# Kernel optimization log

Hardware: AMD Instinct MI355X
Metric: run time of the kernel (lower is better)

Reference implementation:

```python
import jax, jax.numpy as jnp
import numpy as np

HIDDEN = 256
OUT_CH = 3
OMEGA_0 = 30.0
PATCH = 5


def setup_inputs() -> dict:
    key = jax.random.key(0)
    ks = jax.random.split(key, 9)
    B, C, H, W = 1, 128, 256, 256
    in_dim = C * PATCH * PATCH + 2  # 3202
    xi = jax.random.normal(ks[0], (B, C, H, W), dtype=jnp.float32)

    def lin(kw, kb, fi, fo):
        s = 1.0 / np.sqrt(fi)
        Wm = jax.random.uniform(kw, (fi, fo), jnp.float32, -s, s)
        bm = jax.random.uniform(kb, (fo,), jnp.float32, -s, s)
        return Wm, bm

    W1, b1 = lin(ks[1], ks[2], in_dim, HIDDEN)
    W2, b2 = lin(ks[3], ks[4], HIDDEN, HIDDEN)
    W3, b3 = lin(ks[5], ks[6], HIDDEN, HIDDEN)
    W4, b4 = lin(ks[7], ks[8], HIDDEN, OUT_CH)
    return {"xi": xi, "W1": W1, "b1": b1, "W2": W2, "b2": b2,
            "W3": W3, "b3": b3, "W4": W4, "b4": b4}


def _make_coords(B, H, W, dtype):
    # normalized pixel coords in [-1, 1], shape [B*H*W, 2]
    ys = jnp.linspace(-1.0, 1.0, H, dtype=dtype)
    xs = jnp.linspace(-1.0, 1.0, W, dtype=dtype)
    gy, gx = jnp.meshgrid(ys, xs, indexing="ij")
    coords = jnp.stack([gy, gx], axis=-1).reshape(H * W, 2)
    return jnp.tile(coords, (B, 1))


def reference(xi, W1, b1, W2, b2, W3, b3, W4, b4):
    B, C, H, W = xi.shape
    # im2col 5x5 patch gather (zero pad), like F.unfold with padding=2
    patches = jax.lax.conv_general_dilated_patches(
        xi, (PATCH, PATCH), (1, 1), "SAME")  # [B, C*25, H, W]
    feat = jnp.transpose(patches, (0, 2, 3, 1)).reshape(B * H * W, C * PATCH * PATCH)
    coords = _make_coords(B, H, W, xi.dtype)
    x = jnp.concatenate([feat, coords], axis=-1)  # [N, 3202]
    h = jnp.sin(OMEGA_0 * (x @ W1 + b1))
    h = jnp.sin(OMEGA_0 * (h @ W2 + b2))
    h = jnp.sin(OMEGA_0 * (h @ W3 + b3))
    out = h @ W4 + b4  # [N, 3]
    rgb = out.reshape(B, H, W, OUT_CH).transpose(0, 3, 1, 2)
    return rgb
```

## Files before the change

kernel.cpp:

```cpp
#include <hip/hip_runtime.h>
#include <math.h>
#include <stdint.h>

typedef _Float16 f16;
typedef _Float16 f16x8 __attribute__((ext_vector_type(8)));
typedef float f32x4 __attribute__((ext_vector_type(4)));
typedef unsigned short u16;
typedef u16 u16x8 __attribute__((ext_vector_type(8)));

#define HID 256
#define NS1C 100
#define NS2 8
#define NPX 65536
#define BPXG 256
#define NBG (NPX/BPXG)
#define SPAD 260
#define NSP (SPAD*SPAD)

#define OFF_W1C 0
#define SZ_W1C  ((size_t)NS1C*32768)
#define OFF_W2  SZ_W1C
#define SZ_W2   ((size_t)NS2*32768)
#define OFF_W3  (OFF_W2+SZ_W2)
#define OFF_XH  ((size_t)4194304)
#define SZ_XP   ((size_t)NSP*128*2)
#define OFF_XL  (OFF_XH + SZ_XP)
#define OFF_HH  (OFF_XL + SZ_XP)
#define SZ_HP   ((size_t)NPX*HID*2)
#define OFF_HL  (OFF_HH + SZ_HP)

__device__ inline void split2(float v, u16& h, u16& l){
  f16 hv = (f16)v;
  f16 lv = (f16)(v - (float)hv);
  h = __builtin_bit_cast(u16, hv);
  l = __builtin_bit_cast(u16, lv);
}

__global__ void prep_w(const float* __restrict__ W, int Kact, int nStages,
                       u16* __restrict__ outp){
  int t = blockIdx.x*256 + threadIdx.x;
  if (t >= nStages*1024) return;
  int s = t >> 10, r = t & 1023;
  int w = r >> 8, nf = (r >> 6) & 3, l = r & 63;
  int col = w*64 + nf*16 + (l & 15);
  int kb  = s*32 + (l >> 4)*8;
  u16x8 hv, lv;
  #pragma unroll
  for (int j = 0; j < 8; ++j){
    int k = kb + j;
    float v = (k < Kact) ? W[(size_t)k*HID + col] : 0.f;
    u16 h, lo; split2(v, h, lo);
    hv[j] = h; lv[j] = lo;
  }
  size_t U0 = ((((size_t)s*4 + w)*4 + nf)*2 + 0)*64 + l;
  *(u16x8*)(outp + U0*8)      = hv;
  *(u16x8*)(outp + (U0+64)*8) = lv;
}

__global__ void prep_w1c(const float* __restrict__ W1, u16* __restrict__ outp){
  int t = blockIdx.x*256 + threadIdx.x;
  if (t >= NS1C*1024) return;
  int s = t >> 10, r = t & 1023;
  int w = r >> 8, nf = (r >> 6) & 3, l = r & 63;
  int col = w*64 + nf*16 + (l & 15);
  int tap = s >> 2, cg = s & 3;
  int cb  = cg*32 + (l >> 4)*8;
  u16x8 hv, lv;
  #pragma unroll
  for (int j = 0; j < 8; ++j){
    int c = cb + j;
    float v = W1[(size_t)(c*25 + tap)*HID + col];
    u16 h, lo; split2(v, h, lo);
    hv[j] = h; lv[j] = lo;
  }
  size_t U0 = ((((size_t)s*4 + w)*4 + nf)*2 + 0)*64 + l;
  *(u16x8*)(outp + U0*8)      = hv;
  *(u16x8*)(outp + (U0+64)*8) = lv;
}

__global__ __launch_bounds__(256)
void prep_x(const float* __restrict__ xi, u16* __restrict__ Xh, u16* __restrict__ Xl){
  int sp = blockIdx.x*256 + threadIdx.x;
  if (sp >= NSP) return;
  int py = sp / SPAD;
  int px = sp - py*SPAD;
  bool inb = (py >= 2) & (py < 258) & (px >= 2) & (px < 258);
  const float* xin = xi + ((size_t)(py-2)<<8) + (px-2);
  #pragma unroll 4
  for (int cg = 0; cg < 16; ++cg){
    u16x8 hv, lv;
    #pragma unroll
    for (int j = 0; j < 8; ++j){
      float v = inb ? xin[((size_t)(cg*8 + j))<<16] : 0.f;
      u16 h, l; split2(v, h, l); hv[j] = h; lv[j] = l;
    }
    *(u16x8*)(Xh + (size_t)sp*128 + cg*8) = hv;
    *(u16x8*)(Xl + (size_t)sp*128 + cg*8) = lv;
  }
}

template<int MODE>
__global__ __launch_bounds__(512, 2)
void gemm(const u16* __restrict__ Ah, const u16* __restrict__ Al,
          const u16* __restrict__ Wp, const float* __restrict__ W1,
          const float* __restrict__ bias, u16* __restrict__ Hh, u16* __restrict__ Hl,
          const float* __restrict__ W4, const float* __restrict__ b4,
          float* __restrict__ out, int nt)
{
  __shared__ __align__(16) u16 Sb[65536];

  const int tid  = threadIdx.x;
  const int lane = tid & 63;
  const int wv   = tid >> 6;
  const int wm   = wv >> 2, wn = wv & 3;

  int bid = blockIdx.x;
  bid = (bid & 7)*(NBG/8) + (bid >> 3);
  const int pxb = bid * BPXG;
  const int y   = bid;

  f32x4 acc[8][4];
  #pragma unroll
  for (int a=0;a<8;a++)
    #pragma unroll
    for (int bq=0;bq<4;bq++) acc[a][bq] = f32x4{0.f,0.f,0.f,0.f};

#define A_STAGE(S, BUF) do { \
    _Pragma("unroll") \
    for (int u=0;u<2;++u){ \
      const int mfb = wv*2 + u; \
      size_t off; \
      if (MODE == 0){ \
        const int tap = (S) >> 2, cg = (S) & 3; \
        const int dy = tap/5, dx = tap - 5*dy; \
        const int sp = (y + dy)*SPAD + dx + mfb*16 + (lane & 15); \
        off = (size_t)sp*128 + cg*32 + (lane >> 4)*8; \
      } else { \
        const int px = pxb + mfb*16 + (lane & 15); \
        off = (size_t)px*HID + (S)*32 + (lane >> 4)*8; \
      } \
      __builtin_amdgcn_global_load_lds( \
        (const __attribute__((address_space(1))) uint32_t*)(Ah + off), \
        (__attribute__((address_space(3))) uint32_t*)((char*)Sb + (size_t)(BUF)*32768 + (mfb*2+0)*1024), \
        16, 0, 0); \
      __builtin_amdgcn_global_load_lds( \
        (const __attribute__((address_space(1))) uint32_t*)(Al + off), \
        (__attribute__((address_space(3))) uint32_t*)((char*)Sb + (size_t)(BUF)*32768 + (mfb*2+1)*1024), \
        16, 0, 0); \
    } \
  } while(0)

#define B_STAGE(S, BUF) do { \
    const char* _src = (const char*)Wp + (size_t)(S)*32768 + wv*4096 + lane*16; \
    char* _dst = (char*)Sb + 65536 + (size_t)(BUF)*32768 + wv*4096; \
    _Pragma("unroll") \
    for (int i=0;i<4;++i) \
      __builtin_amdgcn_global_load_lds( \
        (const __attribute__((address_space(1))) uint32_t*)(_src + i*1024), \
        (__attribute__((address_space(3))) uint32_t*)(_dst + i*1024), 16, 0, 0); \
  } while(0)

  A_STAGE(0, 0); B_STAGE(0, 0);

  for (int t = 0; t < nt; ++t){
    asm volatile("s_waitcnt vmcnt(0)" ::: "memory");
    __builtin_amdgcn_s_barrier();
    __builtin_amdgcn_sched_barrier(0);
    const int cur = t & 1;
    if (t+1 < nt){
      A_STAGE(t+1, cur^1);
      B_STAGE(t+1, cur^1);
    }

    const u16* Abuf = (const u16*)Sb + (size_t)cur*16384;
    const u16* Bbuf = (const u16*)Sb + 32768 + (size_t)cur*16384;

    f16x8 bh[4], bl[4];
    #pragma unroll
    for (int nf=0;nf<4;++nf){
      bh[nf] = *(const f16x8*)(Bbuf + ((size_t)((wn*4+nf)*2+0)*64 + lane)*8);
      bl[nf] = *(const f16x8*)(Bbuf + ((size_t)((wn*4+nf)*2+1)*64 + lane)*8);
    }
    __builtin_amdgcn_s_setprio(1);
    #pragma unroll
    for (int hf=0; hf<2; ++hf){
      f16x8 ahv[4], alv[4];
      #pragma unroll
      for (int m=0;m<4;++m){
        const int mfb = wm*8 + hf*4 + m;
        ahv[m] = *(const f16x8*)(Abuf + ((size_t)(mfb*2+0)*64 + lane)*8);
        alv[m] = *(const f16x8*)(Abuf + ((size_t)(mfb*2+1)*64 + lane)*8);
      }
      #pragma unroll
      for (int m=0;m<4;++m)
        #pragma unroll
        for (int nf=0;nf<4;++nf)
          acc[hf*4+m][nf] = __builtin_amdgcn_mfma_f32_16x16x32_f16(ahv[m], bh[nf], acc[hf*4+m][nf], 0,0,0);
      #pragma unroll
      for (int m=0;m<4;++m)
        #pragma unroll
        for (int nf=0;nf<4;++nf)
          acc[hf*4+m][nf] = __builtin_amdgcn_mfma_f32_16x16x32_f16(alv[m], bh[nf], acc[hf*4+m][nf], 0,0,0);
      #pragma unroll
      for (int m=0;m<4;++m)
        #pragma unroll
        for (int nf=0;nf<4;++nf)
          acc[hf*4+m][nf] = __builtin_amdgcn_mfma_f32_16x16x32_f16(ahv[m], bl[nf], acc[hf*4+m][nf], 0,0,0);
    }
    __builtin_amdgcn_s_setprio(0);
  }

  __syncthreads();

  float bcol[4];
  #pragma unroll
  for (int nf=0;nf<4;++nf) bcol[nf] = bias[wn*64 + nf*16 + (lane&15)];

  if (MODE == 0){
    float wyv[4], wxv[4];
    #pragma unroll
    for (int nf=0;nf<4;++nf){
      int col = wn*64 + nf*16 + (lane&15);
      wyv[nf] = W1[(size_t)3200*HID + col];
      wxv[nf] = W1[(size_t)3201*HID + col];
    }
    const float gy = -1.f + (2.f/255.f)*(float)y;
    #pragma unroll
    for (int mf=0;mf<8;++mf)
      #pragma unroll
      for (int nf=0;nf<4;++nf)
        #pragma unroll
        for (int j=0;j<4;++j){
          int row = wm*128 + mf*16 + (lane>>4)*4 + j;
          float gx = -1.f + (2.f/255.f)*(float)row;
          float z = acc[mf][nf][j] + bcol[nf] + gy*wyv[nf] + gx*wxv[nf];
          float h = sinf(30.f*z);
          u16 hh,ll; split2(h,hh,ll);
          int col = wn*64 + nf*16 + (lane&15);
          size_t o = (size_t)(pxb+row)*HID + col;
          Hh[o] = hh; Hl[o] = ll;
        }
  } else if (MODE == 1){
    #pragma unroll
    for (int mf=0;mf<8;++mf)
      #pragma unroll
      for (int nf=0;nf<4;++nf)
        #pragma unroll
        for (int j=0;j<4;++j){
          float z = acc[mf][nf][j] + bcol[nf];
          float h = sinf(30.f*z);
          u16 hh,ll; split2(h,hh,ll);
          int row = wm*128 + mf*16 + (lane>>4)*4 + j;
          int col = wn*64 + nf*16 + (lane&15);
          size_t o = (size_t)(pxb+row)*HID + col;
          Hh[o] = hh; Hl[o] = ll;
        }
  } else {
    float (*red)[BPXG][3] = (float(*)[BPXG][3])(void*)Sb;
    float w4v[4][3];
    #pragma unroll
    for (int nf=0;nf<4;++nf){
      int col = wn*64 + nf*16 + (lane&15);
      w4v[nf][0]=W4[col*3+0]; w4v[nf][1]=W4[col*3+1]; w4v[nf][2]=W4[col*3+2];
    }
    #pragma unroll
    for (int mf=0;mf<8;++mf)
      #pragma unroll
      for (int j=0;j<4;++j){
        float s0=0.f,s1=0.f,s2=0.f;
        #pragma unroll
        for (int nf=0;nf<4;++nf){
          float h = sinf(30.f*(acc[mf][nf][j] + bcol[nf]));
          s0 += h*w4v[nf][0]; s1 += h*w4v[nf][1]; s2 += h*w4v[nf][2];
        }
        #pragma unroll
        for (int m=1;m<16;m<<=1){
          s0 += __shfl_xor(s0, m);
          s1 += __shfl_xor(s1, m);
          s2 += __shfl_xor(s2, m);
        }
        if ((lane & 15) == 0){
          int row = wm*128 + mf*16 + (lane>>4)*4 + j;
          red[wn + wm*4][row][0]=s0; red[wn + wm*4][row][1]=s1; red[wn + wm*4][row][2]=s2;
        }
      }
    __syncthreads();
    for (int o = tid; o < BPXG*3; o += 512){
      int px = o & 255, c = o >> 8;
      int wb = (px >> 7)*4;
      float v = red[wb+0][px][c]+red[wb+1][px][c]+red[wb+2][px][c]+red[wb+3][px][c] + b4[c];
      out[(size_t)c*NPX + pxb + px] = v;
    }
  }
#undef A_STAGE
#undef B_STAGE
}

extern "C" void kernel_launch(void* const* d_in, const int* in_sizes, int n_in,
                              void* d_out, int out_size, void* d_ws, size_t ws_size,
                              hipStream_t stream) {
  const float* xi = (const float*)d_in[0];
  const float* W1 = (const float*)d_in[1];
  const float* b1 = (const float*)d_in[2];
  const float* W2 = (const float*)d_in[3];
  const float* b2 = (const float*)d_in[4];
  const float* W3 = (const float*)d_in[5];
  const float* b3 = (const float*)d_in[6];
  const float* W4 = (const float*)d_in[7];
  const float* b4 = (const float*)d_in[8];
  float* out = (float*)d_out;

  char* ws = (char*)d_ws;
  u16* W1c = (u16*)(ws + OFF_W1C);
  u16* W2p = (u16*)(ws + OFF_W2);
  u16* W3p = (u16*)(ws + OFF_W3);
  u16* Xh  = (u16*)(ws + OFF_XH);
  u16* Xl  = (u16*)(ws + OFF_XL);
  u16* Hh  = (u16*)(ws + OFF_HH);
  u16* Hl  = (u16*)(ws + OFF_HL);

  prep_w1c<<<NS1C*4, 256, 0, stream>>>(W1, W1c);
  prep_w<<<NS2*4, 256, 0, stream>>>(W2, HID, NS2, W2p);
  prep_w<<<NS2*4, 256, 0, stream>>>(W3, HID, NS2, W3p);
  prep_x<<<(NSP + 255)/256, 256, 0, stream>>>(xi, Xh, Xl);

  dim3 grid(NBG), block(512);
  gemm<0><<<grid, block, 0, stream>>>(Xh, Xl, W1c, W1, b1, Hh, Hl,
                                      nullptr, nullptr, nullptr, NS1C);
  gemm<1><<<grid, block, 0, stream>>>(Hh, Hl, W2p, nullptr, b2, Hh, Hl,
                                      nullptr, nullptr, nullptr, NS2);
  gemm<2><<<grid, block, 0, stream>>>(Hh, Hl, W3p, nullptr, b3, nullptr, nullptr,
                                      W4, b4, out, NS2);
}
```

Baseline: 471.1 us.

## Merge prep kernels into one launch and fuse layers 2-3 into a single GEMM kernel

The four preprocessing kernels become one launch that dispatches on block index. The layer-2 and layer-3 GEMMs plus the final projection run in one kernel. Layer-2 activations go to a separate workspace buffer and are read back by the same block after a barrier, which works because each block only consumes the rows it produced. This removes launch gaps and tail effects between kernels. It costs extra workspace and a longer-running kernel.

```diff
diff --git a/kernel.cpp b/kernel.cpp
--- a/kernel.cpp
+++ b/kernel.cpp
@@ -28,6 +28,8 @@
 #define OFF_HH  (OFF_XL + SZ_XP)
 #define SZ_HP   ((size_t)NPX*HID*2)
 #define OFF_HL  (OFF_HH + SZ_HP)
+#define OFF_H2H (OFF_HL + SZ_HP)
+#define OFF_H2L (OFF_H2H + SZ_HP)
 
 __device__ inline void split2(float v, u16& h, u16& l){
   f16 hv = (f16)v;
@@ -36,10 +38,8 @@
   l = __builtin_bit_cast(u16, lv);
 }
 
-__global__ void prep_w(const float* __restrict__ W, int Kact, int nStages,
-                       u16* __restrict__ outp){
-  int t = blockIdx.x*256 + threadIdx.x;
-  if (t >= nStages*1024) return;
+__device__ inline void prep_w_body(const float* __restrict__ W, int Kact,
+                                   u16* __restrict__ outp, int t){
   int s = t >> 10, r = t & 1023;
   int w = r >> 8, nf = (r >> 6) & 3, l = r & 63;
   int col = w*64 + nf*16 + (l & 15);
@@ -57,9 +57,8 @@
   *(u16x8*)(outp + (U0+64)*8) = lv;
 }
 
-__global__ void prep_w1c(const float* __restrict__ W1, u16* __restrict__ outp){
-  int t = blockIdx.x*256 + threadIdx.x;
-  if (t >= NS1C*1024) return;
+__device__ inline void prep_w1c_body(const float* __restrict__ W1,
+                                     u16* __restrict__ outp, int t){
   int s = t >> 10, r = t & 1023;
   int w = r >> 8, nf = (r >> 6) & 3, l = r & 63;
   int col = w*64 + nf*16 + (l & 15);
@@ -78,9 +77,9 @@
   *(u16x8*)(outp + (U0+64)*8) = lv;
 }
 
-__global__ __launch_bounds__(256)
-void prep_x(const float* __restrict__ xi, u16* __restrict__ Xh, u16* __restrict__ Xl){
-  int sp = blockIdx.x*256 + threadIdx.x;
+__device__ inline void prep_x_body(const float* __restrict__ xi,
+                                   u16* __restrict__ Xh, u16* __restrict__ Xl,
+                                   int sp){
   if (sp >= NSP) return;
   int py = sp / SPAD;
   int px = sp - py*SPAD;
@@ -99,13 +98,27 @@
   }
 }
 
-template<int MODE>
+__global__ __launch_bounds__(256)
+void prep_all(const float* __restrict__ xi, const float* __restrict__ W1,
+              const float* __restrict__ W2, const float* __restrict__ W3,
+              u16* __restrict__ W1c, u16* __restrict__ W2p, u16* __restrict__ W3p,
+              u16* __restrict__ Xh, u16* __restrict__ Xl){
+  int bid = blockIdx.x, tid = threadIdx.x;
+  if (bid < 400){
+    prep_w1c_body(W1, W1c, bid*256 + tid);
+  } else if (bid < 432){
+    prep_w_body(W2, HID, W2p, (bid-400)*256 + tid);
+  } else if (bid < 464){
+    prep_w_body(W3, HID, W3p, (bid-432)*256 + tid);
+  } else {
+    prep_x_body(xi, Xh, Xl, (bid-464)*256 + tid);
+  }
+}
+
 __global__ __launch_bounds__(512, 2)
-void gemm(const u16* __restrict__ Ah, const u16* __restrict__ Al,
-          const u16* __restrict__ Wp, const float* __restrict__ W1,
-          const float* __restrict__ bias, u16* __restrict__ Hh, u16* __restrict__ Hl,
-          const float* __restrict__ W4, const float* __restrict__ b4,
-          float* __restrict__ out, int nt)
+void gemm_l1(const u16* __restrict__ Xh, const u16* __restrict__ Xl,
+             const u16* __restrict__ Wp, const float* __restrict__ W1,
+             const float* __restrict__ b1, u16* __restrict__ Hh, u16* __restrict__ Hl)
 {
   __shared__ __align__(16) u16 Sb[65536];
 
@@ -129,22 +142,16 @@
     _Pragma("unroll") \
     for (int u=0;u<2;++u){ \
       const int mfb = wv*2 + u; \
-      size_t off; \
-      if (MODE == 0){ \
-        const int tap = (S) >> 2, cg = (S) & 3; \
-        const int dy = tap/5, dx = tap - 5*dy; \
-        const int sp = (y + dy)*SPAD + dx + mfb*16 + (lane & 15); \
-        off = (size_t)sp*128 + cg*32 + (lane >> 4)*8; \
-      } else { \
-        const int px = pxb + mfb*16 + (lane & 15); \
-        off = (size_t)px*HID + (S)*32 + (lane >> 4)*8; \
-      } \
-      __builtin_amdgcn_global_load_lds( \
-        (const __attribute__((address_space(1))) uint32_t*)(Ah + off), \
+      const int tap = (S) >> 2, cg = (S) & 3; \
+      const int dy = tap/5, dx = tap - 5*dy; \
+      const int sp = (y + dy)*SPAD + dx + mfb*16 + (lane & 15); \
+      size_t off = (size_t)sp*128 + cg*32 + (lane >> 4)*8; \
+      __builtin_amdgcn_global_load_lds( \
+        (const __attribute__((address_space(1))) uint32_t*)(Xh + off), \
         (__attribute__((address_space(3))) uint32_t*)((char*)Sb + (size_t)(BUF)*32768 + (mfb*2+0)*1024), \
         16, 0, 0); \
       __builtin_amdgcn_global_load_lds( \
-        (const __attribute__((address_space(1))) uint32_t*)(Al + off), \
+        (const __attribute__((address_space(1))) uint32_t*)(Xl + off), \
         (__attribute__((address_space(3))) uint32_t*)((char*)Sb + (size_t)(BUF)*32768 + (mfb*2+1)*1024), \
         16, 0, 0); \
     } \
@@ -162,12 +169,12 @@
 
   A_STAGE(0, 0); B_STAGE(0, 0);
 
-  for (int t = 0; t < nt; ++t){
+  for (int t = 0; t < NS1C; ++t){
     asm volatile("s_waitcnt vmcnt(0)" ::: "memory");
     __builtin_amdgcn_s_barrier();
     __builtin_amdgcn_sched_barrier(0);
     const int cur = t & 1;
-    if (t+1 < nt){
+    if (t+1 < NS1C){
       A_STAGE(t+1, cur^1);
       B_STAGE(t+1, cur^1);
     }
@@ -209,38 +216,138 @@
     }
     __builtin_amdgcn_s_setprio(0);
   }
-
-  __syncthreads();
-
-  float bcol[4];
+#undef A_STAGE
+#undef B_STAGE
+
+  float bcol[4], wyv[4], wxv[4];
   #pragma unroll
-  for (int nf=0;nf<4;++nf) bcol[nf] = bias[wn*64 + nf*16 + (lane&15)];
-
-  if (MODE == 0){
-    float wyv[4], wxv[4];
-    #pragma unroll
-    for (int nf=0;nf<4;++nf){
-      int col = wn*64 + nf*16 + (lane&15);
-      wyv[nf] = W1[(size_t)3200*HID + col];
-      wxv[nf] = W1[(size_t)3201*HID + col];
-    }
-    const float gy = -1.f + (2.f/255.f)*(float)y;
-    #pragma unroll
-    for (int mf=0;mf<8;++mf)
-      #pragma unroll
-      for (int nf=0;nf<4;++nf)
-        #pragma unroll
-        for (int j=0;j<4;++j){
-          int row = wm*128 + mf*16 + (lane>>4)*4 + j;
-          float gx = -1.f + (2.f/255.f)*(float)row;
-          float z = acc[mf][nf][j] + bcol[nf] + gy*wyv[nf] + gx*wxv[nf];
-          float h = sinf(30.f*z);
-          u16 hh,ll; split2(h,hh,ll);
-          int col = wn*64 + nf*16 + (lane&15);
-          size_t o = (size_t)(pxb+row)*HID + col;
-          Hh[o] = hh; Hl[o] = ll;
-        }
-  } else if (MODE == 1){
+  for (int nf=0;nf<4;++nf){
+    int col = wn*64 + nf*16 + (lane&15);
+    bcol[nf] = b1[col];
+    wyv[nf]  = W1[(size_t)3200*HID + col];
+    wxv[nf]  = W1[(size_t)3201*HID + col];
+  }
+  const float gy = -1.f + (2.f/255.f)*(float)y;
+  #pragma unroll
+  for (int mf=0;mf<8;++mf)
+    #pragma unroll
+    for (int nf=0;nf<4;++nf)
+      #pragma unroll
+      for (int j=0;j<4;++j){
+        int row = wm*128 + mf*16 + (lane>>4)*4 + j;
+        float gx = -1.f + (2.f/255.f)*(float)row;
+        float z = acc[mf][nf][j] + bcol[nf] + gy*wyv[nf] + gx*wxv[nf];
+        float h = sinf(30.f*z);
+        u16 hh,ll; split2(h,hh,ll);
+        int col = wn*64 + nf*16 + (lane&15);
+        size_t o = (size_t)(pxb+row)*HID + col;
+        Hh[o] = hh; Hl[o] = ll;
+      }
+}
+
+__global__ __launch_bounds__(512, 2)
+void gemm_tail(const u16* __restrict__ Hh, const u16* __restrict__ Hl,
+               const u16* __restrict__ W2p, const float* __restrict__ b2,
+               u16* __restrict__ H2h, u16* __restrict__ H2l,
+               const u16* __restrict__ W3p, const float* __restrict__ b3,
+               const float* __restrict__ W4, const float* __restrict__ b4,
+               float* __restrict__ out)
+{
+  __shared__ __align__(16) u16 Sb[65536];
+
+  const int tid  = threadIdx.x;
+  const int lane = tid & 63;
+  const int wv   = tid >> 6;
+  const int wm   = wv >> 2, wn = wv & 3;
+
+  int bid = blockIdx.x;
+  bid = (bid & 7)*(NBG/8) + (bid >> 3);
+  const int pxb = bid * BPXG;
+
+  f32x4 acc[8][4];
+
+#define T_ASTAGE(AHp, ALp, S, BUF) do { \
+    _Pragma("unroll") \
+    for (int u=0;u<2;++u){ \
+      const int mfb = wv*2 + u; \
+      const int px = pxb + mfb*16 + (lane & 15); \
+      size_t off = (size_t)px*HID + (S)*32 + (lane >> 4)*8; \
+      __builtin_amdgcn_global_load_lds( \
+        (const __attribute__((address_space(1))) uint32_t*)((AHp) + off), \
+        (__attribute__((address_space(3))) uint32_t*)((char*)Sb + (size_t)(BUF)*32768 + (mfb*2+0)*1024), \
+        16, 0, 0); \
+      __builtin_amdgcn_global_load_lds( \
+        (const __attribute__((address_space(1))) uint32_t*)((ALp) + off), \
+        (__attribute__((address_space(3))) uint32_t*)((char*)Sb + (size_t)(BUF)*32768 + (mfb*2+1)*1024), \
+        16, 0, 0); \
+    } \
+  } while(0)
+
+#define T_BSTAGE(WPp, S, BUF) do { \
+    const char* _src = (const char*)(WPp) + (size_t)(S)*32768 + wv*4096 + lane*16; \
+    char* _dst = (char*)Sb + 65536 + (size_t)(BUF)*32768 + wv*4096; \
+    _Pragma("unroll") \
+    for (int i=0;i<4;++i) \
+      __builtin_amdgcn_global_load_lds( \
+        (const __attribute__((address_space(1))) uint32_t*)(_src + i*1024), \
+        (__attribute__((address_space(3))) uint32_t*)(_dst + i*1024), 16, 0, 0); \
+  } while(0)
+
+#define T_LOOP(AHp, ALp, WPp) do { \
+    _Pragma("unroll") \
+    for (int a=0;a<8;a++) \
+      _Pragma("unroll") \
+      for (int bq=0;bq<4;bq++) acc[a][bq] = f32x4{0.f,0.f,0.f,0.f}; \
+    T_ASTAGE(AHp, ALp, 0, 0); T_BSTAGE(WPp, 0, 0); \
+    for (int t = 0; t < NS2; ++t){ \
+      asm volatile("s_waitcnt vmcnt(0)" ::: "memory"); \
+      __builtin_amdgcn_s_barrier(); \
+      __builtin_amdgcn_sched_barrier(0); \
+      const int cur = t & 1; \
+      if (t+1 < NS2){ T_ASTAGE(AHp, ALp, t+1, cur^1); T_BSTAGE(WPp, t+1, cur^1); } \
+      const u16* Abuf = (const u16*)Sb + (size_t)cur*16384; \
+      const u16* Bbuf = (const u16*)Sb + 32768 + (size_t)cur*16384; \
+      f16x8 bh[4], bl[4]; \
+      _Pragma("unroll") \
+      for (int nf=0;nf<4;++nf){ \
+        bh[nf] = *(const f16x8*)(Bbuf + ((size_t)((wn*4+nf)*2+0)*64 + lane)*8); \
+        bl[nf] = *(const f16x8*)(Bbuf + ((size_t)((wn*4+nf)*2+1)*64 + lane)*8); \
+      } \
+      __builtin_amdgcn_s_setprio(1); \
+      _Pragma("unroll") \
+      for (int hf=0; hf<2; ++hf){ \
+        f16x8 ahv[4], alv[4]; \
+        _Pragma("unroll") \
+        for (int m=0;m<4;++m){ \
+          const int mfb = wm*8 + hf*4 + m; \
+          ahv[m] = *(const f16x8*)(Abuf + ((size_t)(mfb*2+0)*64 + lane)*8); \
+          alv[m] = *(const f16x8*)(Abuf + ((size_t)(mfb*2+1)*64 + lane)*8); \
+        } \
+        _Pragma("unroll") \
+        for (int m=0;m<4;++m) \
+          _Pragma("unroll") \
+          for (int nf=0;nf<4;++nf) \
+            acc[hf*4+m][nf] = __builtin_amdgcn_mfma_f32_16x16x32_f16(ahv[m], bh[nf], acc[hf*4+m][nf], 0,0,0); \
+        _Pragma("unroll") \
+        for (int m=0;m<4;++m) \
+          _Pragma("unroll") \
+          for (int nf=0;nf<4;++nf) \
+            acc[hf*4+m][nf] = __builtin_amdgcn_mfma_f32_16x16x32_f16(alv[m], bh[nf], acc[hf*4+m][nf], 0,0,0); \
+        _Pragma("unroll") \
+        for (int m=0;m<4;++m) \
+          _Pragma("unroll") \
+          for (int nf=0;nf<4;++nf) \
+            acc[hf*4+m][nf] = __builtin_amdgcn_mfma_f32_16x16x32_f16(ahv[m], bl[nf], acc[hf*4+m][nf], 0,0,0); \
+      } \
+      __builtin_amdgcn_s_setprio(0); \
+    } \
+  } while(0)
+
+  T_LOOP(Hh, Hl, W2p);
+  {
+    float bcol[4];
+    #pragma unroll
+    for (int nf=0;nf<4;++nf) bcol[nf] = b2[wn*64 + nf*16 + (lane&15)];
     #pragma unroll
     for (int mf=0;mf<8;++mf)
       #pragma unroll
@@ -253,9 +360,20 @@
           int row = wm*128 + mf*16 + (lane>>4)*4 + j;
           int col = wn*64 + nf*16 + (lane&15);
           size_t o = (size_t)(pxb+row)*HID + col;
-          Hh[o] = hh; Hl[o] = ll;
+          H2h[o] = hh; H2l[o] = ll;
         }
-  } else {
+  }
+  asm volatile("s_waitcnt vmcnt(0)" ::: "memory");
+  __syncthreads();
+
+  T_LOOP(H2h, H2l, W3p);
+
+  __syncthreads();
+
+  {
+    float bcol[4];
+    #pragma unroll
+    for (int nf=0;nf<4;++nf) bcol[nf] = b3[wn*64 + nf*16 + (lane&15)];
     float (*red)[BPXG][3] = (float(*)[BPXG][3])(void*)Sb;
     float w4v[4][3];
     #pragma unroll
@@ -292,8 +410,9 @@
       out[(size_t)c*NPX + pxb + px] = v;
     }
   }
-#undef A_STAGE
-#undef B_STAGE
+#undef T_ASTAGE
+#undef T_BSTAGE
+#undef T_LOOP
 }
 
 extern "C" void kernel_launch(void* const* d_in, const int* in_sizes, int n_in,
@@ -318,17 +437,13 @@
   u16* Xl  = (u16*)(ws + OFF_XL);
   u16* Hh  = (u16*)(ws + OFF_HH);
   u16* Hl  = (u16*)(ws + OFF_HL);
-
-  prep_w1c<<<NS1C*4, 256, 0, stream>>>(W1, W1c);
-  prep_w<<<NS2*4, 256, 0, stream>>>(W2, HID, NS2, W2p);
-  prep_w<<<NS2*4, 256, 0, stream>>>(W3, HID, NS2, W3p);
-  prep_x<<<(NSP + 255)/256, 256, 0, stream>>>(xi, Xh, Xl);
-
-  dim3 grid(NBG), block(512);
-  gemm<0><<<grid, block, 0, stream>>>(Xh, Xl, W1c, W1, b1, Hh, Hl,
-                                      nullptr, nullptr, nullptr, NS1C);
-  gemm<1><<<grid, block, 0, stream>>>(Hh, Hl, W2p, nullptr, b2, Hh, Hl,
-                                      nullptr, nullptr, nullptr, NS2);
-  gemm<2><<<grid, block, 0, stream>>>(Hh, Hl, W3p, nullptr, b3, nullptr, nullptr,
-                                      W4, b4, out, NS2);
-}
+  u16* H2h = (u16*)(ws + OFF_H2H);
+  u16* H2l = (u16*)(ws + OFF_H2L);
+
+  prep_all<<<729, 256, 0, stream>>>(xi, W1, W2, W3, W1c, W2p, W3p, Xh, Xl);
+
+  gemm_l1<<<NBG, 512, 0, stream>>>(Xh, Xl, W1c, W1, b1, Hh, Hl);
+
+  gemm_tail<<<NBG, 512, 0, stream>>>(Hh, Hl, W2p, b2, H2h, H2l,
+                                     W3p, b3, W4, b4, out);
+}
```

Result: slower. 485.8 us (+3.1%).

## Merge prep kernels into one launch and read B fragments before prefetch

Applied to the files above, without the earlier changes.

The four preprocessing kernels (W1 repack, W2/W3 repack, padded input split) are combined into one kernel that dispatches on block index, which removes three launches and lets the independent work run concurrently. In the GEMM main loop, the B-fragment LDS reads are moved ahead of issuing the next stage's async global-to-LDS loads, with a sched_barrier separating them, so the register loads are not queued behind the new prefetch traffic. Grid size 729 covers 400+32+32+265 blocks, matching the old launch grids.

```diff
diff --git a/kernel.cpp b/kernel.cpp
--- a/kernel.cpp
+++ b/kernel.cpp
@@ -36,10 +36,8 @@
   l = __builtin_bit_cast(u16, lv);
 }
 
-__global__ void prep_w(const float* __restrict__ W, int Kact, int nStages,
-                       u16* __restrict__ outp){
-  int t = blockIdx.x*256 + threadIdx.x;
-  if (t >= nStages*1024) return;
+__device__ inline void prep_w_body(const float* __restrict__ W, int Kact,
+                                   u16* __restrict__ outp, int t){
   int s = t >> 10, r = t & 1023;
   int w = r >> 8, nf = (r >> 6) & 3, l = r & 63;
   int col = w*64 + nf*16 + (l & 15);
@@ -57,9 +55,8 @@
   *(u16x8*)(outp + (U0+64)*8) = lv;
 }
 
-__global__ void prep_w1c(const float* __restrict__ W1, u16* __restrict__ outp){
-  int t = blockIdx.x*256 + threadIdx.x;
-  if (t >= NS1C*1024) return;
+__device__ inline void prep_w1c_body(const float* __restrict__ W1,
+                                     u16* __restrict__ outp, int t){
   int s = t >> 10, r = t & 1023;
   int w = r >> 8, nf = (r >> 6) & 3, l = r & 63;
   int col = w*64 + nf*16 + (l & 15);
@@ -78,9 +75,9 @@
   *(u16x8*)(outp + (U0+64)*8) = lv;
 }
 
-__global__ __launch_bounds__(256)
-void prep_x(const float* __restrict__ xi, u16* __restrict__ Xh, u16* __restrict__ Xl){
-  int sp = blockIdx.x*256 + threadIdx.x;
+__device__ inline void prep_x_body(const float* __restrict__ xi,
+                                   u16* __restrict__ Xh, u16* __restrict__ Xl,
+                                   int sp){
   if (sp >= NSP) return;
   int py = sp / SPAD;
   int px = sp - py*SPAD;
@@ -96,6 +93,23 @@
     }
     *(u16x8*)(Xh + (size_t)sp*128 + cg*8) = hv;
     *(u16x8*)(Xl + (size_t)sp*128 + cg*8) = lv;
+  }
+}
+
+__global__ __launch_bounds__(256)
+void prep_all(const float* __restrict__ xi, const float* __restrict__ W1,
+              const float* __restrict__ W2, const float* __restrict__ W3,
+              u16* __restrict__ W1c, u16* __restrict__ W2p, u16* __restrict__ W3p,
+              u16* __restrict__ Xh, u16* __restrict__ Xl){
+  int bid = blockIdx.x, tid = threadIdx.x;
+  if (bid < 400){
+    prep_w1c_body(W1, W1c, bid*256 + tid);
+  } else if (bid < 432){
+    prep_w_body(W2, HID, W2p, (bid-400)*256 + tid);
+  } else if (bid < 464){
+    prep_w_body(W3, HID, W3p, (bid-432)*256 + tid);
+  } else {
+    prep_x_body(xi, Xh, Xl, (bid-464)*256 + tid);
   }
 }
 
@@ -167,20 +181,22 @@
     __builtin_amdgcn_s_barrier();
     __builtin_amdgcn_sched_barrier(0);
     const int cur = t & 1;
+
+    const u16* Abuf = (const u16*)Sb + (size_t)cur*16384;
+    const u16* Bbuf = (const u16*)Sb + 32768 + (size_t)cur*16384;
+
+    f16x8 bh[4], bl[4];
+    #pragma unroll
+    for (int nf=0;nf<4;++nf){
+      bh[nf] = *(const f16x8*)(Bbuf + ((size_t)((wn*4+nf)*2+0)*64 + lane)*8);
+      bl[nf] = *(const f16x8*)(Bbuf + ((size_t)((wn*4+nf)*2+1)*64 + lane)*8);
+    }
+    __builtin_amdgcn_sched_barrier(0);
     if (t+1 < nt){
       A_STAGE(t+1, cur^1);
       B_STAGE(t+1, cur^1);
     }
 
-    const u16* Abuf = (const u16*)Sb + (size_t)cur*16384;
-    const u16* Bbuf = (const u16*)Sb + 32768 + (size_t)cur*16384;
-
-    f16x8 bh[4], bl[4];
-    #pragma unroll
-    for (int nf=0;nf<4;++nf){
-      bh[nf] = *(const f16x8*)(Bbuf + ((size_t)((wn*4+nf)*2+0)*64 + lane)*8);
-      bl[nf] = *(const f16x8*)(Bbuf + ((size_t)((wn*4+nf)*2+1)*64 + lane)*8);
-    }
     __builtin_amdgcn_s_setprio(1);
     #pragma unroll
     for (int hf=0; hf<2; ++hf){
@@ -319,10 +335,7 @@
   u16* Hh  = (u16*)(ws + OFF_HH);
   u16* Hl  = (u16*)(ws + OFF_HL);
 
-  prep_w1c<<<NS1C*4, 256, 0, stream>>>(W1, W1c);
-  prep_w<<<NS2*4, 256, 0, stream>>>(W2, HID, NS2, W2p);
-  prep_w<<<NS2*4, 256, 0, stream>>>(W3, HID, NS2, W3p);
-  prep_x<<<(NSP + 255)/256, 256, 0, stream>>>(xi, Xh, Xl);
+  prep_all<<<729, 256, 0, stream>>>(xi, W1, W2, W3, W1c, W2p, W3p, Xh, Xl);
 
   dim3 grid(NBG), block(512);
   gemm<0><<<grid, block, 0, stream>>>(Xh, Xl, W1c, W1, b1, Hh, Hl,
```

After: 459.4 us. -2.5%, faster.
